# Kernel tuning notes

Measured on AMD Instinct MI355X. Metric: run time of the kernel, lower is better.

The kernel has to match this reference:

```python
import jax, jax.numpy as jnp
import numpy as np

N_NODES = 100000
N_EDGES = 1600000
NODE_DIM = 32
EDGE_DIM = 8
NUM_LAYERS = 3
NEG_SLOPE = 0.01  # F.leaky_relu default
EPS = 0.0         # GINEConv default eps, train_eps=False


def setup_inputs() -> dict:
    key = jax.random.key(0)
    ks = jax.random.split(key, 7)
    x = jax.random.normal(ks[0], (N_NODES, NODE_DIM), dtype=jnp.float32)
    edge_attr = jax.random.normal(ks[1], (N_EDGES, EDGE_DIM), dtype=jnp.float32)
    W = jax.random.normal(ks[2], (NUM_LAYERS, NODE_DIM, NODE_DIM), dtype=jnp.float32) / np.sqrt(NODE_DIM)
    b = jax.random.normal(ks[3], (NUM_LAYERS, NODE_DIM), dtype=jnp.float32) * 0.01
    We = jax.random.normal(ks[4], (NUM_LAYERS, EDGE_DIM, NODE_DIM), dtype=jnp.float32) / np.sqrt(EDGE_DIM)
    be = jax.random.normal(ks[5], (NUM_LAYERS, NODE_DIM), dtype=jnp.float32) * 0.01
    edge_index = jax.random.randint(ks[6], (2, N_EDGES), 0, N_NODES, dtype=jnp.int64 if jax.config.jax_enable_x64 else jnp.int32)
    return {"x": x, "edge_attr": edge_attr, "W": W, "b": b, "We": We, "be": be,
            "edge_index": edge_index}


def reference(x, edge_attr, W, b, We, be, edge_index):
    # 3 stacked GINEConv layers + leaky_relu, PyG semantics:
    # out = Linear((1+eps)*x_i + sum_{j->i} ReLU(x_j + Lin_e(edge_attr_ji)))
    src = edge_index[0]  # source nodes j
    dst = edge_index[1]  # target nodes i
    n = x.shape[0]
    for l in range(NUM_LAYERS):
        e = edge_attr @ We[l] + be[l]                       # [E, D] edge embedding
        msg = jax.nn.relu(x[src] + e)                        # gather + message
        agg = jax.ops.segment_sum(msg, dst, num_segments=n)  # scatter-add
        h = (1.0 + EPS) * x + agg
        x = jax.nn.leaky_relu(h @ W[l] + b[l], negative_slope=NEG_SLOPE)
    return x
```

## Files before the change

### kernel.cpp

```cpp
#include <hip/hip_runtime.h>

#define N_NODES 100000
#define N_EDGES 1600000
#define D 32
#define ED 8
#define NEG_SLOPE 0.01f
#define BSH 9
#define BKN 512
#define CB ((N_NODES + BKN - 1) / BKN)
#define FB_SPLIT 2
#define A_EPB 1024
#define A_NB ((N_EDGES + A_EPB - 1) / A_EPB)
#define NBLK 98

typedef unsigned int uint;
typedef unsigned short ushort;
typedef __fp16 half2v __attribute__((ext_vector_type(2)));

__device__ __forceinline__ uint bf16_rne(float f) {
    uint u = __float_as_uint(f);
    return (u + 0x7fffu + ((u >> 16) & 1u)) >> 16;
}
__device__ __forceinline__ uint pack2(float lo, float hi) {
    return bf16_rne(lo) | (bf16_rne(hi) << 16);
}
__device__ __forceinline__ float bf_lo(uint u) { return __uint_as_float(u << 16); }
__device__ __forceinline__ float bf_hi(uint u) { return __uint_as_float(u & 0xffff0000u); }
__device__ __forceinline__ float bf_us(ushort u) { return __uint_as_float(((uint)u) << 16); }

__device__ __forceinline__ uint ph2(float lo, float hi) {
    __fp16 l = (__fp16)lo, h = (__fp16)hi;
    return (uint)__builtin_bit_cast(ushort, l) | ((uint)__builtin_bit_cast(ushort, h) << 16);
}

#if defined(__has_builtin) && __has_builtin(__builtin_amdgcn_fdot2)
__device__ __forceinline__ float fdot2f(uint u, half2v w, float c) {
    return __builtin_amdgcn_fdot2(__builtin_bit_cast(half2v, u), w, c, false);
}
#else
__device__ __forceinline__ float fdot2f(uint u, half2v w, float c) {
    half2v a = __builtin_bit_cast(half2v, u);
    return c + (float)a.x * (float)w.x + (float)a.y * (float)w.y;
}
#endif

__global__ __launch_bounds__(256) void pack_x_kernel(
    const float* __restrict__ x, ushort* __restrict__ xb)
{
    int i = blockIdx.x * 256 + threadIdx.x;
    if (i >= N_NODES * D / 4) return;
    float4 f = ((const float4*)x)[i];
    ((uint2*)xb)[i] = make_uint2(pack2(f.x, f.y), pack2(f.z, f.w));
}

__global__ __launch_bounds__(256) void countA_kernel(
    const int* __restrict__ dst, int* __restrict__ cntM)
{
    __shared__ int h[CB];
    const int t = threadIdx.x;
    for (int i = t; i < CB; i += 256) h[i] = 0;
    __syncthreads();
    const int e0 = blockIdx.x * A_EPB;
    for (int j = 0; j < A_EPB; j += 256) {
        int e = e0 + j + t;
        if (e < N_EDGES) atomicAdd(&h[dst[e] >> BSH], 1);
    }
    __syncthreads();
    for (int i = t; i < CB; i += 256) cntM[blockIdx.x * CB + i] = h[i];
}

__global__ __launch_bounds__(1024) void scanS1_kernel(
    const int* __restrict__ cntM, int* __restrict__ exclM, int* __restrict__ btot)
{
    __shared__ int s[1024];
    const int t = threadIdx.x;
    const int b = blockIdx.x;
    const int r0 = 2 * t, r1 = 2 * t + 1;
    int v0 = (r0 < A_NB) ? cntM[r0 * CB + b] : 0;
    int v1 = (r1 < A_NB) ? cntM[r1 * CB + b] : 0;
    s[t] = v0 + v1;
    __syncthreads();
    for (int off = 1; off < 1024; off <<= 1) {
        int u = (t >= off) ? s[t - off] : 0;
        __syncthreads();
        s[t] += u;
        __syncthreads();
    }
    int base0 = s[t] - v0 - v1;
    if (r0 < A_NB) exclM[r0 * CB + b] = base0;
    if (r1 < A_NB) exclM[r1 * CB + b] = base0 + v0;
    if (t == 1023) btot[b] = s[1023];
}

__global__ __launch_bounds__(1024) void scanS2_kernel(
    const int* __restrict__ btot, int* __restrict__ bbase, int* __restrict__ row_ptr)
{
    __shared__ int s[1024];
    const int t = threadIdx.x;
    int v = (t < CB) ? btot[t] : 0;
    s[t] = v;
    __syncthreads();
    for (int off = 1; off < 1024; off <<= 1) {
        int u = (t >= off) ? s[t - off] : 0;
        __syncthreads();
        s[t] += u;
        __syncthreads();
    }
    if (t < CB) bbase[t] = s[t] - v;
    if (t == 0) row_ptr[N_NODES] = N_EDGES;
}

__global__ __launch_bounds__(256) void scatterA_kernel(
    const int*   __restrict__ src,
    const int*   __restrict__ dst,
    const float* __restrict__ edge_attr,
    const int*   __restrict__ exclM,
    const int*   __restrict__ bbase,
    uint4*       __restrict__ ea_tmp,
    uint*        __restrict__ sd_tmp)
{
    __shared__ int cur[CB];
    const int t = threadIdx.x;
    for (int i = t; i < CB; i += 256)
        cur[i] = bbase[i] + exclM[blockIdx.x * CB + i];
    __syncthreads();
    const int e0 = blockIdx.x * A_EPB;
    const float4* ea4 = (const float4*)edge_attr;
    for (int j = 0; j < A_EPB; j += 256) {
        int e = e0 + j + t;
        if (e >= N_EDGES) continue;
        int dn = dst[e];
        int pos = atomicAdd(&cur[dn >> BSH], 1);
        float4 a = ea4[(long)e * 2];
        float4 c = ea4[(long)e * 2 + 1];
        ea_tmp[pos] = make_uint4(ph2(a.x, a.y), ph2(a.z, a.w),
                                 ph2(c.x, c.y), ph2(c.z, c.w));
        sd_tmp[pos] = (uint)src[e] | ((uint)(dn & (BKN - 1)) << 20);
    }
}

__global__ __launch_bounds__(512) void fineB_kernel(
    const uint4* __restrict__ ea_tmp,
    const uint*  __restrict__ sd_tmp,
    const int*   __restrict__ bbase,
    int*         __restrict__ row_ptr,
    uint4*       __restrict__ ea16,
    int*         __restrict__ srcf)
{
    __shared__ int h[BKN];
    __shared__ int ex[BKN];
    const int t = threadIdx.x;
    const int b = blockIdx.x / FB_SPLIT;
    const int s = blockIdx.x % FB_SPLIT;
    const int e0 = bbase[b];
    const int e1 = (b == CB - 1) ? N_EDGES : bbase[b + 1];

    h[t] = 0;
    __syncthreads();
    for (int r = e0 + t; r < e1; r += 512)
        atomicAdd(&h[sd_tmp[r] >> 20], 1);
    __syncthreads();
    ex[t] = h[t];
    __syncthreads();
    for (int off = 1; off < BKN; off <<= 1) {
        int u = (t >= off) ? ex[t - off] : 0;
        __syncthreads();
        ex[t] += u;
        __syncthreads();
    }
    {
        int excl = ex[t] - h[t];
        int n = b * BKN + t;
        if (s == 0 && n < N_NODES) row_ptr[n] = e0 + excl;
        h[t] = e0 + excl;
    }
    __syncthreads();
    for (int r = e0 + t; r < e1; r += 512) {
        uint sd = sd_tmp[r];
        int nl = (int)(sd >> 20);
        if ((nl >> 8) == s) {
            uint4 ea = ea_tmp[r];
            int pos = atomicAdd(&h[nl], 1);
            ea16[pos] = ea;
            srcf[pos] = (int)(sd & 0xFFFFFu);
        }
    }
}

__global__ __launch_bounds__(256) void gine_fused4_kernel(
    const ushort* __restrict__ xb_in, ushort* __restrict__ xb_out,
    float* __restrict__ f32_out, const int* __restrict__ row_ptr,
    const uint4* __restrict__ ea16, const int* __restrict__ srcf,
    const float* __restrict__ W, const float* __restrict__ b,
    const float* __restrict__ We, const float* __restrict__ be)
{
    __shared__ float W_s[D * D];
    const int t = threadIdx.x;
    for (int i = t; i < D * D; i += 256) W_s[i] = W[i];

    const int n = blockIdx.x * 8 + (t >> 5);
    const int d = t & 31;

    half2v wep[4];
#pragma unroll
    for (int k = 0; k < 4; ++k) {
        wep[k].x = (__fp16)We[(2 * k) * D + d];
        wep[k].y = (__fp16)We[(2 * k + 1) * D + d];
    }
    const float bed = be[d];
    const float bd  = b[d];
    __syncthreads();
    if (n >= N_NODES) return;

    const int row = row_ptr[n], rend = row_ptr[n + 1];
    float selfx = bf_us(xb_in[n * D + d]);

    float acc = 0.0f;
    for (int base = row; base < rend; base += 16) {
        const int nrem = rend - base;
        const int lid = d & 15;
        const int sidx = base + ((lid < nrem) ? lid : (nrem - 1));
        const int svec = srcf[sidx];
        uint xu[16];
#pragma unroll
        for (int j = 0; j < 16; ++j) {
            int sj = __shfl(svec, j, 32);
            xu[j] = xb_in[sj * D + d];
        }
#pragma unroll
        for (int c = 0; c < 4; ++c) {
            if (4 * c >= nrem) break;
            uint4 ev[4];
#pragma unroll
            for (int j = 0; j < 4; ++j) {
                int idx = base + 4 * c + j;
                ev[j] = ea16[(idx < rend) ? idx : (rend - 1)];
            }
#pragma unroll
            for (int j = 0; j < 4; ++j) {
                int idx = base + 4 * c + j;
                float e = fdot2f(ev[j].w, wep[3],
                          fdot2f(ev[j].z, wep[2],
                          fdot2f(ev[j].y, wep[1],
                          fdot2f(ev[j].x, wep[0], bed))));
                float msg = fmaxf(bf_us((ushort)xu[4 * c + j]) + e, 0.0f);
                acc += (idx < rend) ? msg : 0.0f;
            }
        }
    }

    float h = selfx + acc;
    float o = bd;
#pragma unroll
    for (int k = 0; k < D; ++k)
        o += __shfl(h, k, 32) * W_s[k * D + d];
    o = o > 0.0f ? o : NEG_SLOPE * o;
    xb_out[n * D + d] = (ushort)bf16_rne(o);
    if (f32_out) f32_out[n * D + d] = o;
}

__global__ __launch_bounds__(256) void hist_kernel(
    const int* __restrict__ dst, int* __restrict__ deg)
{
    int i = blockIdx.x * 256 + threadIdx.x;
    if (i >= N_EDGES / 4) return;
    int4 dd = ((const int4*)dst)[i];
    atomicAdd(&deg[dd.x], 1);
    atomicAdd(&deg[dd.y], 1);
    atomicAdd(&deg[dd.z], 1);
    atomicAdd(&deg[dd.w], 1);
}

__global__ __launch_bounds__(1024) void scan_phase1(
    const int* __restrict__ deg, int* __restrict__ bsums)
{
    __shared__ int s[1024];
    int t = threadIdx.x;
    int i = blockIdx.x * 1024 + t;
    s[t] = (i < N_NODES) ? deg[i] : 0;
    __syncthreads();
    for (int off = 512; off > 0; off >>= 1) {
        if (t < off) s[t] += s[t + off];
        __syncthreads();
    }
    if (t == 0) bsums[blockIdx.x] = s[0];
}

__global__ __launch_bounds__(128) void scan_phase2(int* __restrict__ bsums)
{
    __shared__ int s[128];
    int t = threadIdx.x;
    int v = (t < NBLK) ? bsums[t] : 0;
    s[t] = v;
    __syncthreads();
    for (int off = 1; off < 128; off <<= 1) {
        int u = (t >= off) ? s[t - off] : 0;
        __syncthreads();
        s[t] += u;
        __syncthreads();
    }
    if (t < NBLK) bsums[t] = s[t] - v;
}

__global__ __launch_bounds__(1024) void scan_phase3(
    const int* __restrict__ deg, const int* __restrict__ bsums,
    int* __restrict__ row_ptr, int* __restrict__ offs)
{
    __shared__ int s[1024];
    int t = threadIdx.x;
    int i = blockIdx.x * 1024 + t;
    int v = (i < N_NODES) ? deg[i] : 0;
    s[t] = v;
    __syncthreads();
    for (int off = 1; off < 1024; off <<= 1) {
        int u = (t >= off) ? s[t - off] : 0;
        __syncthreads();
        s[t] += u;
        __syncthreads();
    }
    int excl = bsums[blockIdx.x] + s[t] - v;
    if (i < N_NODES) { row_ptr[i] = excl; offs[i] = excl; }
    else if (i == N_NODES) row_ptr[i] = excl;
}

__global__ __launch_bounds__(256) void scatter_rec_kernel(
    const int* __restrict__ src, const int* __restrict__ dst,
    const float* __restrict__ edge_attr, int* __restrict__ offs,
    uint* __restrict__ rec)
{
    int e = blockIdx.x * 256 + threadIdx.x;
    if (e >= N_EDGES) return;
    int pos = atomicAdd(&offs[dst[e]], 1);
    const float4* ea4 = (const float4*)edge_attr;
    float4 a = ea4[(long)e * 2];
    float4 c = ea4[(long)e * 2 + 1];
    uint* r = rec + (long)pos * 8;
    *(uint4*)r = make_uint4((uint)src[e], pack2(a.x, a.y), pack2(a.z, a.w), pack2(c.x, c.y));
    r[4] = pack2(c.z, c.w);
}

__global__ __launch_bounds__(256) void gine_fused2_kernel(
    const ushort* __restrict__ xb_in, ushort* __restrict__ xb_out,
    float* __restrict__ f32_out, const int* __restrict__ row_ptr,
    const uint* __restrict__ rec,
    const float* __restrict__ W, const float* __restrict__ b,
    const float* __restrict__ We, const float* __restrict__ be)
{
    __shared__ float W_s[D * D];
    __shared__ float We_s[ED * D];
    __shared__ float b_s[D];
    __shared__ float be_s[D];
    const int t = threadIdx.x;
    for (int i = t; i < D * D; i += 256) W_s[i] = W[i];
    if (t < ED * D) We_s[t] = We[t];
    if (t < D) { b_s[t] = b[t]; be_s[t] = be[t]; }
    __syncthreads();
    const int n = blockIdx.x * 8 + (t >> 5);
    const int d = t & 31;
    if (n >= N_NODES) return;
    float wer[ED];
#pragma unroll
    for (int k = 0; k < ED; ++k) wer[k] = We_s[k * D + d];
    const float bed = be_s[d];
    const int row = row_ptr[n], rend = row_ptr[n + 1];
    float selfx = bf_us(xb_in[n * D + d]);
    float acc = 0.0f;
    for (int pos = row; pos < rend; pos += 8) {
        const int rem = rend - pos;
        const uint2* rp = (const uint2*)(rec + (long)pos * 8);
        uint2 v = rp[d];
        int srcs[8];
#pragma unroll
        for (int j = 0; j < 8; ++j) srcs[j] = __shfl((int)v.x, 4 * j, 32);
        const int s0 = srcs[0];
        float xv[8];
#pragma unroll
        for (int j = 0; j < 8; ++j) {
            int sj = (j < rem) ? srcs[j] : s0;
            xv[j] = bf_us(xb_in[sj * D + d]);
        }
#pragma unroll
        for (int j = 0; j < 8; ++j) {
            uint u01 = (uint)__shfl((int)v.y, 4 * j, 32);
            uint u23 = (uint)__shfl((int)v.x, 4 * j + 1, 32);
            uint u45 = (uint)__shfl((int)v.y, 4 * j + 1, 32);
            uint u67 = (uint)__shfl((int)v.x, 4 * j + 2, 32);
            float e = bed;
            e += bf_lo(u01) * wer[0]; e += bf_hi(u01) * wer[1];
            e += bf_lo(u23) * wer[2]; e += bf_hi(u23) * wer[3];
            e += bf_lo(u45) * wer[4]; e += bf_hi(u45) * wer[5];
            e += bf_lo(u67) * wer[6]; e += bf_hi(u67) * wer[7];
            float msg = fmaxf(xv[j] + e, 0.0f);
            acc += (j < rem) ? msg : 0.0f;
        }
    }
    float h = selfx + acc;
    float o = b_s[d];
#pragma unroll
    for (int k = 0; k < D; ++k)
        o += __shfl(h, k, 32) * W_s[k * D + d];
    o = o > 0.0f ? o : NEG_SLOPE * o;
    xb_out[n * D + d] = (ushort)bf16_rne(o);
    if (f32_out) f32_out[n * D + d] = o;
}

__global__ __launch_bounds__(256) void gine_edge_kernel(
    const float* __restrict__ x, const float* __restrict__ edge_attr,
    const float* __restrict__ We, const float* __restrict__ be,
    const int* __restrict__ src, const int* __restrict__ dst,
    float* __restrict__ agg)
{
    __shared__ float We_s[ED * D];
    __shared__ float be_s[D];
    int t = threadIdx.x;
    if (t < ED * D) We_s[t] = We[t];
    if (t < D) be_s[t] = be[t];
    __syncthreads();
    long gtid = (long)blockIdx.x * blockDim.x + t;
    int e = (int)(gtid >> 5), d = (int)(gtid & 31);
    if (e >= N_EDGES) return;
    int s = src[e], dn = dst[e];
    float acc = be_s[d];
#pragma unroll
    for (int k = 0; k < ED; ++k)
        acc += edge_attr[(long)e * ED + k] * We_s[k * D + d];
    float m = fmaxf(x[(long)s * D + d] + acc, 0.0f);
    atomicAdd(&agg[(long)dn * D + d], m);
}

__global__ __launch_bounds__(256) void gine_node_kernel(
    float* __restrict__ x, const float* __restrict__ agg,
    const float* __restrict__ W, const float* __restrict__ b)
{
    __shared__ float W_s[D * D];
    __shared__ float b_s[D];
    int t = threadIdx.x;
    for (int i = t; i < D * D; i += 256) W_s[i] = W[i];
    if (t < D) b_s[t] = b[t];
    __syncthreads();
    long gtid = (long)blockIdx.x * blockDim.x + t;
    int n = (int)(gtid >> 5), d = (int)(gtid & 31);
    if (n >= N_NODES) return;
    float h = x[(long)n * D + d] + agg[(long)n * D + d];
    float acc = b_s[d];
#pragma unroll
    for (int k = 0; k < D; ++k)
        acc += __shfl(h, k, D) * W_s[k * D + d];
    x[(long)n * D + d] = acc > 0.0f ? acc : NEG_SLOPE * acc;
}

extern "C" void kernel_launch(void* const* d_in, const int* in_sizes, int n_in,
                              void* d_out, int out_size, void* d_ws, size_t ws_size,
                              hipStream_t stream) {
    const float* x_in      = (const float*)d_in[0];
    const float* edge_attr = (const float*)d_in[1];
    const float* W         = (const float*)d_in[2];
    const float* b         = (const float*)d_in[3];
    const float* We        = (const float*)d_in[4];
    const float* be        = (const float*)d_in[5];
    const int*   ei        = (const int*)d_in[6];
    const int* src = ei;
    const int* dst = ei + N_EDGES;

    const size_t xbytes  = (size_t)N_NODES * D * sizeof(float);
    const size_t xbbytes = (size_t)N_NODES * D * sizeof(ushort);

    auto align = [](size_t v) { return (v + 255) & ~(size_t)255; };
    size_t off_xba  = 0;
    size_t off_rp   = align(off_xba + xbbytes);
    size_t off_cnt  = align(off_rp + (N_NODES + 1) * sizeof(int));
    size_t off_excl = align(off_cnt + (size_t)A_NB * CB * sizeof(int));
    size_t off_bt   = align(off_excl + (size_t)A_NB * CB * sizeof(int));
    size_t off_bb   = align(off_bt + CB * sizeof(int));
    size_t off_ea   = align(off_bb + CB * sizeof(int));
    size_t off_src  = align(off_ea + ((size_t)N_EDGES + 8) * 16);
    size_t off_eat  = align(off_src + ((size_t)N_EDGES + 8) * 4);
    size_t off_sdt  = align(off_eat + ((size_t)N_EDGES + 8) * 16);
    size_t need_big = off_sdt + ((size_t)N_EDGES + 8) * 4 + 256;
    size_t off_mrec = off_ea;
    size_t off_mxbb = align(off_mrec + ((size_t)N_EDGES + 8) * 32);
    size_t need_mid = off_mxbb + xbbytes + 256;

    char* ws = (char*)d_ws;
    ushort* xbA    = (ushort*)(ws + off_xba);
    int*   row_ptr = (int*)   (ws + off_rp);
    int*   cntM    = (int*)   (ws + off_cnt);
    int*   exclM   = (int*)   (ws + off_excl);
    int*   btot    = (int*)   (ws + off_bt);
    int*   bbase   = (int*)   (ws + off_bb);
    uint4* ea16    = (uint4*) (ws + off_ea);
    int*   srcf    = (int*)   (ws + off_src);
    uint4* ea_tmp  = (uint4*) (ws + off_eat);
    uint*  sd_tmp  = (uint*)  (ws + off_sdt);
    ushort* xbB    = (ushort*)(ws + off_eat);
    float* xout    = (float*)d_out;

    if (ws_size >= need_big) {
        pack_x_kernel<<<(N_NODES * D / 4 + 255) / 256, 256, 0, stream>>>(x_in, xbA);
        countA_kernel<<<A_NB, 256, 0, stream>>>(dst, cntM);
        scanS1_kernel<<<CB, 1024, 0, stream>>>(cntM, exclM, btot);
        scanS2_kernel<<<1, 1024, 0, stream>>>(btot, bbase, row_ptr);
        scatterA_kernel<<<A_NB, 256, 0, stream>>>(src, dst, edge_attr, exclM, bbase,
                                                  ea_tmp, sd_tmp);
        fineB_kernel<<<CB * FB_SPLIT, 512, 0, stream>>>(ea_tmp, sd_tmp, bbase, row_ptr,
                                                        ea16, srcf);

        dim3 blk(256), grid((N_NODES + 7) / 8);
        gine_fused4_kernel<<<grid, blk, 0, stream>>>(xbA, xbB, nullptr, row_ptr, ea16, srcf,
            W, b, We, be);
        gine_fused4_kernel<<<grid, blk, 0, stream>>>(xbB, xbA, nullptr, row_ptr, ea16, srcf,
            W + D * D, b + D, We + ED * D, be + D);
        gine_fused4_kernel<<<grid, blk, 0, stream>>>(xbA, xbB, xout, row_ptr, ea16, srcf,
            W + 2 * D * D, b + 2 * D, We + 2 * ED * D, be + 2 * D);
    } else if (ws_size >= need_mid) {
        int* deg  = cntM;
        int* offs = exclM;
        int* bsums = btot;
        uint* rec = (uint*)(ws + off_mrec);
        ushort* xbBm = (ushort*)(ws + off_mxbb);
        pack_x_kernel<<<(N_NODES * D / 4 + 255) / 256, 256, 0, stream>>>(x_in, xbA);
        hipMemsetAsync(deg, 0, N_NODES * sizeof(int), stream);
        hist_kernel<<<(N_EDGES / 4 + 255) / 256, 256, 0, stream>>>(dst, deg);
        scan_phase1<<<NBLK, 1024, 0, stream>>>(deg, bsums);
        scan_phase2<<<1, 128, 0, stream>>>(bsums);
        scan_phase3<<<NBLK, 1024, 0, stream>>>(deg, bsums, row_ptr, offs);
        scatter_rec_kernel<<<(N_EDGES + 255) / 256, 256, 0, stream>>>(
            src, dst, edge_attr, offs, rec);
        dim3 blk(256), grid((N_NODES + 7) / 8);
        gine_fused2_kernel<<<grid, blk, 0, stream>>>(xbA, xbBm, nullptr, row_ptr, rec,
            W, b, We, be);
        gine_fused2_kernel<<<grid, blk, 0, stream>>>(xbBm, xbA, nullptr, row_ptr, rec,
            W + D * D, b + D, We + ED * D, be + D);
        gine_fused2_kernel<<<grid, blk, 0, stream>>>(xbA, xbBm, xout, row_ptr, rec,
            W + 2 * D * D, b + 2 * D, We + 2 * ED * D, be + 2 * D);
    } else {
        float* x = (float*)d_out;
        float* agg = (float*)d_ws;
        hipMemcpyAsync(x, x_in, xbytes, hipMemcpyDeviceToDevice, stream);
        dim3 eblk(256), egrid(((long)N_EDGES * D + 255) / 256);
        dim3 nblk(256), ngrid(((long)N_NODES * D + 255) / 256);
        for (int l = 0; l < 3; ++l) {
            hipMemsetAsync(agg, 0, xbytes, stream);
            gine_edge_kernel<<<egrid, eblk, 0, stream>>>(
                x, edge_attr, We + (size_t)l * ED * D, be + (size_t)l * D, src, dst, agg);
            gine_node_kernel<<<ngrid, nblk, 0, stream>>>(
                x, agg, W + (size_t)l * D * D, b + (size_t)l * D);
        }
    }
}
```

Baseline: 399.9 us.

## Split fused GINE layer into edge-balanced segment pass and node pass

Replaces the per-node fused gather/aggregate/linear kernel with two kernels per layer. The first splits the CSR edge list into fixed 128-edge segments per half-wavefront, binary-searches row_ptr for the starting node, and flushes per-node partial sums with atomicAdd into an fp32 aggregation buffer. The second applies the self term, the linear layer and leaky_relu, then zeroes the buffer for the next layer. The aim is to remove load imbalance and tail waste from variable node degrees. The cost is an extra fp32 aggregation round trip, atomics, a binary search per segment and three more launches.

```diff
diff --git a/kernel.cpp b/kernel.cpp
--- a/kernel.cpp
+++ b/kernel.cpp
@@ -11,6 +11,7 @@
 #define FB_SPLIT 2
 #define A_EPB 1024
 #define A_NB ((N_EDGES + A_EPB - 1) / A_EPB)
+#define SEG 128
 #define NBLK 98
 
 typedef unsigned int uint;
@@ -187,18 +188,16 @@
     }
 }
 
-__global__ __launch_bounds__(256) void gine_fused4_kernel(
-    const ushort* __restrict__ xb_in, ushort* __restrict__ xb_out,
-    float* __restrict__ f32_out, const int* __restrict__ row_ptr,
-    const uint4* __restrict__ ea16, const int* __restrict__ srcf,
-    const float* __restrict__ W, const float* __restrict__ b,
-    const float* __restrict__ We, const float* __restrict__ be)
-{
-    __shared__ float W_s[D * D];
-    const int t = threadIdx.x;
-    for (int i = t; i < D * D; i += 256) W_s[i] = W[i];
-
-    const int n = blockIdx.x * 8 + (t >> 5);
+__global__ __launch_bounds__(256) void gine_edge_pass(
+    const ushort* __restrict__ xb_in,
+    float* __restrict__ agg,
+    const int* __restrict__ row_ptr,
+    const uint4* __restrict__ ea16,
+    const int* __restrict__ srcf,
+    const float* __restrict__ We,
+    const float* __restrict__ be)
+{
+    const int t = threadIdx.x;
     const int d = t & 31;
 
     half2v wep[4];
@@ -208,55 +207,78 @@
         wep[k].y = (__fp16)We[(2 * k + 1) * D + d];
     }
     const float bed = be[d];
-    const float bd  = b[d];
-    __syncthreads();
-    if (n >= N_NODES) return;
-
-    const int row = row_ptr[n], rend = row_ptr[n + 1];
-    float selfx = bf_us(xb_in[n * D + d]);
+
+    const int hw = blockIdx.x * 8 + (t >> 5);
+    const int s0 = hw * SEG;
+    if (s0 >= N_EDGES) return;
+    const int s1 = (s0 + SEG < N_EDGES) ? (s0 + SEG) : N_EDGES;
+
+    int lo = 0, hi = N_NODES;
+    while (hi - lo > 1) {
+        int mid = (lo + hi) >> 1;
+        if (row_ptr[mid] <= s0) lo = mid; else hi = mid;
+    }
+    int n = lo;
+    int nend = row_ptr[n + 1];
 
     float acc = 0.0f;
-    for (int base = row; base < rend; base += 16) {
-        const int nrem = rend - base;
-        const int lid = d & 15;
-        const int sidx = base + ((lid < nrem) ? lid : (nrem - 1));
-        const int svec = srcf[sidx];
-        uint xu[16];
-#pragma unroll
-        for (int j = 0; j < 16; ++j) {
-            int sj = __shfl(svec, j, 32);
-            xu[j] = xb_in[sj * D + d];
+    for (int base = s0; base < s1; base += 4) {
+        uint4 ev[4];
+        int sj[4];
+#pragma unroll
+        for (int j = 0; j < 4; ++j) {
+            int idx = base + j; idx = (idx < s1) ? idx : (s1 - 1);
+            ev[j] = ea16[idx];
+            sj[j] = srcf[idx];
         }
-#pragma unroll
-        for (int c = 0; c < 4; ++c) {
-            if (4 * c >= nrem) break;
-            uint4 ev[4];
-#pragma unroll
-            for (int j = 0; j < 4; ++j) {
-                int idx = base + 4 * c + j;
-                ev[j] = ea16[(idx < rend) ? idx : (rend - 1)];
-            }
-#pragma unroll
-            for (int j = 0; j < 4; ++j) {
-                int idx = base + 4 * c + j;
-                float e = fdot2f(ev[j].w, wep[3],
-                          fdot2f(ev[j].z, wep[2],
-                          fdot2f(ev[j].y, wep[1],
-                          fdot2f(ev[j].x, wep[0], bed))));
-                float msg = fmaxf(bf_us((ushort)xu[4 * c + j]) + e, 0.0f);
-                acc += (idx < rend) ? msg : 0.0f;
+        float xv[4];
+#pragma unroll
+        for (int j = 0; j < 4; ++j)
+            xv[j] = bf_us(xb_in[sj[j] * D + d]);
+#pragma unroll
+        for (int j = 0; j < 4; ++j) {
+            int e = base + j;
+            if (e < s1) {
+                while (e >= nend) {
+                    if (acc != 0.0f) atomicAdd(&agg[(long)n * D + d], acc);
+                    acc = 0.0f;
+                    ++n;
+                    nend = row_ptr[n + 1];
+                }
+                float ee = fdot2f(ev[j].w, wep[3],
+                           fdot2f(ev[j].z, wep[2],
+                           fdot2f(ev[j].y, wep[1],
+                           fdot2f(ev[j].x, wep[0], bed))));
+                acc += fmaxf(xv[j] + ee, 0.0f);
             }
         }
     }
-
-    float h = selfx + acc;
+    if (acc != 0.0f) atomicAdd(&agg[(long)n * D + d], acc);
+}
+
+__global__ __launch_bounds__(256) void gine_node_pass(
+    const ushort* __restrict__ xb_in, ushort* __restrict__ xb_out,
+    float* __restrict__ f32_out, float* __restrict__ agg,
+    const float* __restrict__ W, const float* __restrict__ b)
+{
+    __shared__ float W_s[D * D];
+    const int t = threadIdx.x;
+    for (int i = t; i < D * D; i += 256) W_s[i] = W[i];
+    const int n = blockIdx.x * 8 + (t >> 5);
+    const int d = t & 31;
+    const float bd = b[d];
+    __syncthreads();
+    if (n >= N_NODES) return;
+    const long off = (long)n * D + d;
+    float h = bf_us(xb_in[off]) + agg[off];
+    agg[off] = 0.0f;
     float o = bd;
 #pragma unroll
     for (int k = 0; k < D; ++k)
         o += __shfl(h, k, 32) * W_s[k * D + d];
     o = o > 0.0f ? o : NEG_SLOPE * o;
-    xb_out[n * D + d] = (ushort)bf16_rne(o);
-    if (f32_out) f32_out[n * D + d] = o;
+    xb_out[off] = (ushort)bf16_rne(o);
+    if (f32_out) f32_out[off] = o;
 }
 
 __global__ __launch_bounds__(256) void hist_kernel(
@@ -464,6 +486,7 @@
 
     const size_t xbytes  = (size_t)N_NODES * D * sizeof(float);
     const size_t xbbytes = (size_t)N_NODES * D * sizeof(ushort);
+    const size_t aggbytes = (size_t)N_NODES * D * sizeof(float);
 
     auto align = [](size_t v) { return (v + 255) & ~(size_t)255; };
     size_t off_xba  = 0;
@@ -477,6 +500,7 @@
     size_t off_eat  = align(off_src + ((size_t)N_EDGES + 8) * 4);
     size_t off_sdt  = align(off_eat + ((size_t)N_EDGES + 8) * 16);
     size_t need_big = off_sdt + ((size_t)N_EDGES + 8) * 4 + 256;
+    size_t off_agg  = align(off_eat + xbbytes);
     size_t off_mrec = off_ea;
     size_t off_mxbb = align(off_mrec + ((size_t)N_EDGES + 8) * 32);
     size_t need_mid = off_mxbb + xbbytes + 256;
@@ -493,6 +517,7 @@
     uint4* ea_tmp  = (uint4*) (ws + off_eat);
     uint*  sd_tmp  = (uint*)  (ws + off_sdt);
     ushort* xbB    = (ushort*)(ws + off_eat);
+    float* agg     = (float*) (ws + off_agg);
     float* xout    = (float*)d_out;
 
     if (ws_size >= need_big) {
@@ -504,14 +529,20 @@
                                                   ea_tmp, sd_tmp);
         fineB_kernel<<<CB * FB_SPLIT, 512, 0, stream>>>(ea_tmp, sd_tmp, bbase, row_ptr,
                                                         ea16, srcf);
-
-        dim3 blk(256), grid((N_NODES + 7) / 8);
-        gine_fused4_kernel<<<grid, blk, 0, stream>>>(xbA, xbB, nullptr, row_ptr, ea16, srcf,
-            W, b, We, be);
-        gine_fused4_kernel<<<grid, blk, 0, stream>>>(xbB, xbA, nullptr, row_ptr, ea16, srcf,
-            W + D * D, b + D, We + ED * D, be + D);
-        gine_fused4_kernel<<<grid, blk, 0, stream>>>(xbA, xbB, xout, row_ptr, ea16, srcf,
-            W + 2 * D * D, b + 2 * D, We + 2 * ED * D, be + 2 * D);
+        hipMemsetAsync(agg, 0, aggbytes, stream);
+
+        const int EGRID = (N_EDGES / SEG + 7) / 8;
+        dim3 blk(256), ngrid((N_NODES + 7) / 8);
+        gine_edge_pass<<<EGRID, blk, 0, stream>>>(xbA, agg, row_ptr, ea16, srcf, We, be);
+        gine_node_pass<<<ngrid, blk, 0, stream>>>(xbA, xbB, nullptr, agg, W, b);
+        gine_edge_pass<<<EGRID, blk, 0, stream>>>(xbB, agg, row_ptr, ea16, srcf,
+            We + ED * D, be + D);
+        gine_node_pass<<<ngrid, blk, 0, stream>>>(xbB, xbA, nullptr, agg,
+            W + D * D, b + D);
+        gine_edge_pass<<<EGRID, blk, 0, stream>>>(xbA, agg, row_ptr, ea16, srcf,
+            We + 2 * ED * D, be + 2 * D);
+        gine_node_pass<<<ngrid, blk, 0, stream>>>(xbA, xbB, xout, agg,
+            W + 2 * D * D, b + 2 * D);
     } else if (ws_size >= need_mid) {
         int* deg  = cntM;
         int* offs = exclM;
@@ -535,16 +566,16 @@
             W + 2 * D * D, b + 2 * D, We + 2 * ED * D, be + 2 * D);
     } else {
         float* x = (float*)d_out;
-        float* agg = (float*)d_ws;
+        float* agg2 = (float*)d_ws;
         hipMemcpyAsync(x, x_in, xbytes, hipMemcpyDeviceToDevice, stream);
         dim3 eblk(256), egrid(((long)N_EDGES * D + 255) / 256);
-        dim3 nblk(256), ngrid(((long)N_NODES * D + 255) / 256);
+        dim3 nblk(256), ngrid2(((long)N_NODES * D + 255) / 256);
         for (int l = 0; l < 3; ++l) {
-            hipMemsetAsync(agg, 0, xbytes, stream);
+            hipMemsetAsync(agg2, 0, xbytes, stream);
             gine_edge_kernel<<<egrid, eblk, 0, stream>>>(
-                x, edge_attr, We + (size_t)l * ED * D, be + (size_t)l * D, src, dst, agg);
-            gine_node_kernel<<<ngrid, nblk, 0, stream>>>(
-                x, agg, W + (size_t)l * D * D, b + (size_t)l * D);
+                x, edge_attr, We + (size_t)l * ED * D, be + (size_t)l * D, src, dst, agg2);
+            gine_node_kernel<<<ngrid2, nblk, 0, stream>>>(
+                x, agg2, W + (size_t)l * D * D, b + (size_t)l * D);
         }
     }
 }
```

Result: slower. 478.8 us (+19.7%).
